# Kernel tuning notes

Hardware: AMD Instinct MI355X
Metric: run time of the kernel (lower is better)

## Reference

```python
import jax, jax.numpy as jnp
import numpy as np

N_HEAD = 16

def setup_inputs() -> dict:
    key = jax.random.key(0)
    k1, k2, k3, k4, k5 = jax.random.split(key, 5)
    B, T, C = 2, 2048, 1024
    scale = 1.0 / np.sqrt(C)
    return {
        "x": jax.random.normal(k1, (B, T, C), dtype=jnp.float32),
        "Wqkv": jax.random.normal(k2, (C, 3 * C), dtype=jnp.float32) * scale,
        "bqkv": jax.random.normal(k3, (3 * C,), dtype=jnp.float32) * 0.02,
        "Wproj": jax.random.normal(k4, (C, C), dtype=jnp.float32) * scale,
        "bproj": jax.random.normal(k5, (C,), dtype=jnp.float32) * 0.02,
    }

def reference(x, Wqkv, bqkv, Wproj, bproj):
    B, T, C = x.shape
    H = N_HEAD
    D = C // H
    # qkv projection, split last dim as (3, H, D): first C cols = q, etc.
    qkv = (x @ Wqkv + bqkv).reshape(B, T, 3, H, D)
    q, k, v = qkv[:, :, 0], qkv[:, :, 1], qkv[:, :, 2]  # (B, T, H, D)
    att = jnp.einsum("bqhd,bkhd->bhqk", q, k) * (1.0 / np.sqrt(D))
    causal = jnp.tril(jnp.ones((T, T), dtype=bool))
    att = jnp.where(causal, att, -jnp.inf)
    att = jax.nn.softmax(att, axis=-1)
    y = jnp.einsum("bhqk,bkhd->bqhd", att, v).reshape(B, T, C)
    return y @ Wproj + bproj
```

## Files before the change

### kernel.cpp

```cpp
#include <hip/hip_runtime.h>
#include <hip/hip_bf16.h>
#include <stdint.h>

typedef unsigned short u16;
typedef __attribute__((ext_vector_type(8))) short bf16x8;
typedef __attribute__((ext_vector_type(4))) float f32x4;

#define MFMA16(a,b,c) __builtin_amdgcn_mfma_f32_16x16x32_bf16((a),(b),(c),0,0,0)

__device__ __forceinline__ u16 f2bf(float f) {
    union { float f; uint32_t u; } v; v.f = f;
    return (u16)((v.u + 0x7FFFu + ((v.u >> 16) & 1u)) >> 16);
}

__global__ void k_convert(const float* __restrict__ in, u16* __restrict__ out) {
    int i = (blockIdx.x * 256 + threadIdx.x) * 4;
    f32x4 v = *(const f32x4*)(in + i);
    uint64_t p = (uint64_t)f2bf(v[0]) | ((uint64_t)f2bf(v[1]) << 16)
               | ((uint64_t)f2bf(v[2]) << 32) | ((uint64_t)f2bf(v[3]) << 48);
    *(uint64_t*)(out + i) = p;
}

__global__ void k_transpose_convert(const float* __restrict__ W, u16* __restrict__ WT,
                                    int R, int NC) {
    int id = blockIdx.x * 256 + threadIdx.x;
    int n = id % NC, kc = id / NC;
    bf16x8 o;
#pragma unroll
    for (int i = 0; i < 8; ++i)
        o[i] = (short)f2bf(W[(size_t)(kc * 8 + i) * NC + n]);
    *(bf16x8*)(WT + (size_t)n * R + kc * 8) = o;
}

__global__ void k_transpose_v(const u16* __restrict__ V, u16* __restrict__ Vt) {
    int id = blockIdx.x * 256 + threadIdx.x;
    int d = id & 63, tc = (id >> 6) & 255, bh = id >> 14;
    const u16* src = V + (size_t)bh * 131072 + d;
    u16* dst = Vt + (size_t)bh * 131072 + (size_t)d * 2048 + tc * 8;
    bf16x8 o;
#pragma unroll
    for (int i = 0; i < 8; ++i) o[i] = (short)src[(size_t)(tc * 8 + i) * 64];
    *(bf16x8*)dst = o;
}

__global__ __launch_bounds__(256, 2) void k_gemm(
    const u16* __restrict__ A, const u16* __restrict__ Bt,
    const float* __restrict__ bias,
    u16* __restrict__ outQKV, float* __restrict__ outF,
    int M, int N, int K, int mode)
{
    __shared__ __align__(16) u16 As[2][128 * 32];
    __shared__ __align__(16) u16 Bs[2][128 * 32];
    const int tid = threadIdx.x;
    const int nbx = N >> 7;
    const int bm = blockIdx.x / nbx, bn = blockIdx.x % nbx;
    const int m0 = bm << 7, n0 = bn << 7;
    const int l = tid & 63, w = tid >> 6;
    const int wr = w >> 1, wc = w & 1;
    const int kl = l >> 4, lr = l & 15;

    const int r0 = tid >> 2, kc0 = tid & 3, r1 = r0 + 64;
    const int wa0 = r0 * 32 + (((kc0 ^ (r0 >> 1)) & 3) << 3);
    const int wa1 = r1 * 32 + (((kc0 ^ (r1 >> 1)) & 3) << 3);
    const size_t ga0 = (size_t)r0 * K + kc0 * 8;
    const size_t ga1 = (size_t)r1 * K + kc0 * 8;
    const u16* Ag = A + (size_t)m0 * K;
    const u16* Bg = Bt + (size_t)n0 * K;

    f32x4 acc[4][4] = {};

    int ra[4], rb[4];
#pragma unroll
    for (int m = 0; m < 4; ++m) {
        int row = wr * 64 + m * 16 + lr;
        ra[m] = row * 32 + (((kl ^ (row >> 1)) & 3) << 3);
    }
#pragma unroll
    for (int n = 0; n < 4; ++n) {
        int row = wc * 64 + n * 16 + lr;
        rb[n] = row * 32 + (((kl ^ (row >> 1)) & 3) << 3);
    }

    {
        bf16x8 a0 = *(const bf16x8*)(Ag + ga0);
        bf16x8 a1 = *(const bf16x8*)(Ag + ga1);
        bf16x8 b0 = *(const bf16x8*)(Bg + ga0);
        bf16x8 b1 = *(const bf16x8*)(Bg + ga1);
        *(bf16x8*)&As[0][wa0] = a0; *(bf16x8*)&As[0][wa1] = a1;
        *(bf16x8*)&Bs[0][wa0] = b0; *(bf16x8*)&Bs[0][wa1] = b1;
    }
    __syncthreads();

    const int nK = K >> 5;
    int cur = 0;
    for (int ks = 0; ks < nK; ++ks) {
        bf16x8 a0, a1, b0, b1;
        const bool pre = (ks + 1 < nK);
        if (pre) {
            size_t off = (size_t)(ks + 1) * 32;
            a0 = *(const bf16x8*)(Ag + ga0 + off);
            a1 = *(const bf16x8*)(Ag + ga1 + off);
            b0 = *(const bf16x8*)(Bg + ga0 + off);
            b1 = *(const bf16x8*)(Bg + ga1 + off);
        }
        bf16x8 af[4], bfr[4];
#pragma unroll
        for (int m = 0; m < 4; ++m) af[m] = *(const bf16x8*)&As[cur][ra[m]];
#pragma unroll
        for (int n = 0; n < 4; ++n) bfr[n] = *(const bf16x8*)&Bs[cur][rb[n]];
#pragma unroll
        for (int m = 0; m < 4; ++m)
#pragma unroll
            for (int n = 0; n < 4; ++n)
                acc[m][n] = MFMA16(af[m], bfr[n], acc[m][n]);
        if (pre) {
            int nxt = cur ^ 1;
            *(bf16x8*)&As[nxt][wa0] = a0; *(bf16x8*)&As[nxt][wa1] = a1;
            *(bf16x8*)&Bs[nxt][wa0] = b0; *(bf16x8*)&Bs[nxt][wa1] = b1;
        }
        __syncthreads();
        cur ^= 1;
    }

    if (mode == 0) {
#pragma unroll
        for (int n = 0; n < 4; ++n) {
            int gn = n0 + wc * 64 + n * 16 + lr;
            float bv = bias[gn];
            int s = gn >> 10, hd = gn & 1023;
            int hh = hd >> 6, dd = hd & 63;
            float mult = (s == 0) ? 0.125f : 1.0f;
            size_t base = (size_t)s * 4194304 + (size_t)hh * 131072 + dd;
#pragma unroll
            for (int m = 0; m < 4; ++m)
#pragma unroll
                for (int j = 0; j < 4; ++j) {
                    int gm = m0 + wr * 64 + m * 16 + kl * 4 + j;
                    int bb = gm >> 11, tt = gm & 2047;
                    float val = (acc[m][n][j] + bv) * mult;
                    outQKV[base + (size_t)bb * 2097152 + (size_t)tt * 64] = f2bf(val);
                }
        }
    } else {
#pragma unroll
        for (int n = 0; n < 4; ++n) {
            int gn = n0 + wc * 64 + n * 16 + lr;
            float bv = bias[gn];
#pragma unroll
            for (int m = 0; m < 4; ++m)
#pragma unroll
                for (int j = 0; j < 4; ++j) {
                    int gm = m0 + wr * 64 + m * 16 + kl * 4 + j;
                    outF[(size_t)gm * N + gn] = acc[m][n][j] + bv;
                }
        }
    }
}

__global__ __launch_bounds__(256, 4) void k_attn(
    const u16* __restrict__ Qg, const u16* __restrict__ Kg,
    const u16* __restrict__ Vtg, u16* __restrict__ Yg)
{
    const int bid = blockIdx.x;
    const int bh = bid & 31;
    const int qt = 31 - (bid >> 5);
    const int b = bh >> 4, h = bh & 15;
    const int q0 = qt << 6;
    const int tid = threadIdx.x, l = tid & 63, w = tid >> 6;
    const int kl = l >> 4, lr = l & 15;

    __shared__ __align__(16) u16 Qs[64 * 64];
    __shared__ __align__(16) u16 Ks[64 * 64];
    __shared__ __align__(16) u16 Vs[64 * 64];
    __shared__ __align__(16) u16 Ps[4][16 * 72];

    const u16* Qb = Qg + (size_t)bh * 131072;
    const u16* Kb = Kg + (size_t)bh * 131072;
    const u16* Vb = Vtg + (size_t)bh * 131072;

    const int rr = tid >> 3, ch = tid & 7;
    {
        bf16x8 a = *(const bf16x8*)(Qb + (size_t)(q0 + rr) * 64 + ch * 8);
        bf16x8 c = *(const bf16x8*)(Qb + (size_t)(q0 + rr + 32) * 64 + ch * 8);
        *(bf16x8*)&Qs[rr * 64 + ((ch ^ (rr & 7)) << 3)] = a;
        *(bf16x8*)&Qs[(rr + 32) * 64 + ((ch ^ (rr & 7)) << 3)] = c;
    }
    __syncthreads();
    bf16x8 qa[2];
#pragma unroll
    for (int kk = 0; kk < 2; ++kk) {
        int row = w * 16 + lr;
        qa[kk] = *(const bf16x8*)&Qs[row * 64 + (((kk * 4 + kl) ^ (row & 7)) << 3)];
    }

    f32x4 oacc[4] = {};
    float lsum[4] = {0.f, 0.f, 0.f, 0.f};

    bf16x8 kv0 = *(const bf16x8*)(Kb + (size_t)rr * 64 + ch * 8);
    bf16x8 kv1 = *(const bf16x8*)(Kb + (size_t)(rr + 32) * 64 + ch * 8);
    bf16x8 vv0 = *(const bf16x8*)(Vb + (size_t)rr * 2048 + ch * 8);
    bf16x8 vv1 = *(const bf16x8*)(Vb + (size_t)(rr + 32) * 2048 + ch * 8);

    for (int kt = 0; kt <= qt; ++kt) {
        const int k0 = kt << 6;
        __syncthreads();
        *(bf16x8*)&Ks[rr * 64 + ((ch ^ (rr & 7)) << 3)] = kv0;
        *(bf16x8*)&Ks[(rr + 32) * 64 + ((ch ^ (rr & 7)) << 3)] = kv1;
        *(bf16x8*)&Vs[rr * 64 + ((ch ^ (rr & 7)) << 3)] = vv0;
        *(bf16x8*)&Vs[(rr + 32) * 64 + ((ch ^ (rr & 7)) << 3)] = vv1;
        __syncthreads();
        if (kt < qt) {
            const int k0n = k0 + 64;
            kv0 = *(const bf16x8*)(Kb + (size_t)(k0n + rr) * 64 + ch * 8);
            kv1 = *(const bf16x8*)(Kb + (size_t)(k0n + rr + 32) * 64 + ch * 8);
            vv0 = *(const bf16x8*)(Vb + (size_t)rr * 2048 + k0n + ch * 8);
            vv1 = *(const bf16x8*)(Vb + (size_t)(rr + 32) * 2048 + k0n + ch * 8);
        }

        f32x4 s[4];
#pragma unroll
        for (int nb = 0; nb < 4; ++nb) {
            f32x4 a = {};
            int key = nb * 16 + lr;
#pragma unroll
            for (int kk = 0; kk < 2; ++kk) {
                bf16x8 kb = *(const bf16x8*)&Ks[key * 64 + (((kk * 4 + kl) ^ (key & 7)) << 3)];
                a = MFMA16(qa[kk], kb, a);
            }
            s[nb] = a;
        }
        if (kt == qt) {
#pragma unroll
            for (int nb = 0; nb < 4; ++nb) {
                int key = k0 + nb * 16 + lr;
#pragma unroll
                for (int j = 0; j < 4; ++j) {
                    int q = q0 + w * 16 + kl * 4 + j;
                    if (key > q) s[nb][j] = -__builtin_inff();
                }
            }
        }
#pragma unroll
        for (int j = 0; j < 4; ++j) {
            float acc4 = 0.f;
#pragma unroll
            for (int nb = 0; nb < 4; ++nb) {
                float p = __expf(s[nb][j]);
                s[nb][j] = p;
                acc4 += p;
            }
            lsum[j] += acc4;
        }
#pragma unroll
        for (int nb = 0; nb < 4; ++nb)
#pragma unroll
            for (int j = 0; j < 4; ++j)
                Ps[w][(kl * 4 + j) * 72 + nb * 16 + lr] = f2bf(s[nb][j]);
        bf16x8 pa[2];
#pragma unroll
        for (int kk = 0; kk < 2; ++kk)
            pa[kk] = *(const bf16x8*)&Ps[w][lr * 72 + kk * 32 + kl * 8];
#pragma unroll
        for (int db = 0; db < 4; ++db) {
            int d = db * 16 + lr;
#pragma unroll
            for (int kk = 0; kk < 2; ++kk) {
                bf16x8 vb = *(const bf16x8*)&Vs[d * 64 + (((kk * 4 + kl) ^ (d & 7)) << 3)];
                oacc[db] = MFMA16(pa[kk], vb, oacc[db]);
            }
        }
    }
#pragma unroll
    for (int j = 0; j < 4; ++j) {
#pragma unroll
        for (int off = 1; off < 16; off <<= 1) lsum[j] += __shfl_xor(lsum[j], off);
        lsum[j] = 1.f / lsum[j];
    }
#pragma unroll
    for (int db = 0; db < 4; ++db)
#pragma unroll
        for (int j = 0; j < 4; ++j) {
            int q = q0 + w * 16 + kl * 4 + j;
            int col = h * 64 + db * 16 + lr;
            Yg[(size_t)(b * 2048 + q) * 1024 + col] = f2bf(oacc[db][j] * lsum[j]);
        }
}

extern "C" void kernel_launch(void* const* d_in, const int* in_sizes, int n_in,
                              void* d_out, int out_size, void* d_ws, size_t ws_size,
                              hipStream_t stream) {
    const float* x     = (const float*)d_in[0];
    const float* Wqkv  = (const float*)d_in[1];
    const float* bqkv  = (const float*)d_in[2];
    const float* Wproj = (const float*)d_in[3];
    const float* bproj = (const float*)d_in[4];
    float* out = (float*)d_out;

    char* ws = (char*)d_ws;
    u16* xb     = (u16*)(ws);
    u16* WqkvT  = (u16*)(ws + 8388608);
    u16* WprojT = (u16*)(ws + 14680064);
    u16* qkv    = (u16*)(ws + 16777216);
    u16* Vt   = xb;
    u16* Yatt = qkv + 2 * 4194304;

    k_convert<<<4096, 256, 0, stream>>>(x, xb);
    k_transpose_convert<<<1536, 256, 0, stream>>>(Wqkv, WqkvT, 1024, 3072);
    k_transpose_convert<<<512, 256, 0, stream>>>(Wproj, WprojT, 1024, 1024);
    k_gemm<<<768, 256, 0, stream>>>(xb, WqkvT, bqkv, qkv, nullptr,
                                    4096, 3072, 1024, 0);
    k_transpose_v<<<2048, 256, 0, stream>>>(qkv + 2 * 4194304, Vt);
    k_attn<<<1024, 256, 0, stream>>>(qkv, qkv + 4194304, Vt, Yatt);
    k_gemm<<<256, 256, 0, stream>>>(Yatt, WprojT, bproj, nullptr, out,
                                    4096, 1024, 1024, 1);
}
```

Measured before the change: 119.8 us.

## Use direct global-to-LDS loads in GEMM and narrow projection tile

The GEMM kernel becomes a template on the number of N-repeats and the output mode. Tiles are now staged with direct global-to-LDS 16-byte loads instead of loading into registers and then storing to LDS. The bank-conflict swizzle moves from the LDS write address to the global read address. The output projection uses a 128x64 tile with twice as many blocks, and both GEMMs declare launch bounds for higher occupancy. The aim is to cut register pressure and VGPR round-trips on the load path and to fill more CUs for the smaller projection GEMM, at the cost of relying on the async LDS load path being ordered correctly by the barriers.

```diff
diff --git a/kernel.cpp b/kernel.cpp
--- a/kernel.cpp
+++ b/kernel.cpp
@@ -43,89 +43,102 @@
     *(bf16x8*)dst = o;
 }
 
-__global__ __launch_bounds__(256, 2) void k_gemm(
+template<int NREP, int MODE>
+__device__ __forceinline__ void gemm_body(
     const u16* __restrict__ A, const u16* __restrict__ Bt,
     const float* __restrict__ bias,
     u16* __restrict__ outQKV, float* __restrict__ outF,
-    int M, int N, int K, int mode)
+    int M, int N, int K)
 {
+    constexpr int BN = 32 * NREP;
+    constexpr int WN = 16 * NREP;
+    constexpr int BSLOTS = NREP / 2;
     __shared__ __align__(16) u16 As[2][128 * 32];
-    __shared__ __align__(16) u16 Bs[2][128 * 32];
+    __shared__ __align__(16) u16 Bs[2][BN * 32];
     const int tid = threadIdx.x;
-    const int nbx = N >> 7;
+    const int nbx = N / BN;
     const int bm = blockIdx.x / nbx, bn = blockIdx.x % nbx;
-    const int m0 = bm << 7, n0 = bn << 7;
+    const int m0 = bm << 7, n0 = bn * BN;
     const int l = tid & 63, w = tid >> 6;
     const int wr = w >> 1, wc = w & 1;
     const int kl = l >> 4, lr = l & 15;
 
-    const int r0 = tid >> 2, kc0 = tid & 3, r1 = r0 + 64;
-    const int wa0 = r0 * 32 + (((kc0 ^ (r0 >> 1)) & 3) << 3);
-    const int wa1 = r1 * 32 + (((kc0 ^ (r1 >> 1)) & 3) << 3);
-    const size_t ga0 = (size_t)r0 * K + kc0 * 8;
-    const size_t ga1 = (size_t)r1 * K + kc0 * 8;
     const u16* Ag = A + (size_t)m0 * K;
     const u16* Bg = Bt + (size_t)n0 * K;
 
-    f32x4 acc[4][4] = {};
-
-    int ra[4], rb[4];
+    int a_src[2], a_dst[2];
+#pragma unroll
+    for (int s = 0; s < 2; ++s) {
+        int cb = w * 128 + s * 64;
+        int c = cb + l;
+        int r = c >> 2, kc = c & 3;
+        a_src[s] = r * K + ((kc ^ ((r >> 1) & 3)) << 3);
+        a_dst[s] = cb << 3;
+    }
+    int b_src[BSLOTS], b_dst[BSLOTS];
+#pragma unroll
+    for (int s = 0; s < BSLOTS; ++s) {
+        int cb = (w * BSLOTS + s) * 64;
+        int c = cb + l;
+        int r = c >> 2, kc = c & 3;
+        b_src[s] = r * K + ((kc ^ ((r >> 1) & 3)) << 3);
+        b_dst[s] = cb << 3;
+    }
+
+    int ra[4], rb[NREP];
 #pragma unroll
     for (int m = 0; m < 4; ++m) {
         int row = wr * 64 + m * 16 + lr;
         ra[m] = row * 32 + (((kl ^ (row >> 1)) & 3) << 3);
     }
 #pragma unroll
-    for (int n = 0; n < 4; ++n) {
-        int row = wc * 64 + n * 16 + lr;
+    for (int n = 0; n < NREP; ++n) {
+        int row = wc * WN + n * 16 + lr;
         rb[n] = row * 32 + (((kl ^ (row >> 1)) & 3) << 3);
     }
 
-    {
-        bf16x8 a0 = *(const bf16x8*)(Ag + ga0);
-        bf16x8 a1 = *(const bf16x8*)(Ag + ga1);
-        bf16x8 b0 = *(const bf16x8*)(Bg + ga0);
-        bf16x8 b1 = *(const bf16x8*)(Bg + ga1);
-        *(bf16x8*)&As[0][wa0] = a0; *(bf16x8*)&As[0][wa1] = a1;
-        *(bf16x8*)&Bs[0][wa0] = b0; *(bf16x8*)&Bs[0][wa1] = b1;
-    }
+    f32x4 acc[4][NREP] = {};
+
+#pragma unroll
+    for (int s = 0; s < 2; ++s)
+        __builtin_amdgcn_global_load_lds(Ag + a_src[s], &As[0][a_dst[s]], 16, 0, 0);
+#pragma unroll
+    for (int s = 0; s < BSLOTS; ++s)
+        __builtin_amdgcn_global_load_lds(Bg + b_src[s], &Bs[0][b_dst[s]], 16, 0, 0);
     __syncthreads();
 
     const int nK = K >> 5;
     int cur = 0;
     for (int ks = 0; ks < nK; ++ks) {
-        bf16x8 a0, a1, b0, b1;
-        const bool pre = (ks + 1 < nK);
-        if (pre) {
-            size_t off = (size_t)(ks + 1) * 32;
-            a0 = *(const bf16x8*)(Ag + ga0 + off);
-            a1 = *(const bf16x8*)(Ag + ga1 + off);
-            b0 = *(const bf16x8*)(Bg + ga0 + off);
-            b1 = *(const bf16x8*)(Bg + ga1 + off);
-        }
-        bf16x8 af[4], bfr[4];
+        if (ks + 1 < nK) {
+            int off = (ks + 1) << 5;
+#pragma unroll
+            for (int s = 0; s < 2; ++s)
+                __builtin_amdgcn_global_load_lds(Ag + a_src[s] + off,
+                                                 &As[cur ^ 1][a_dst[s]], 16, 0, 0);
+#pragma unroll
+            for (int s = 0; s < BSLOTS; ++s)
+                __builtin_amdgcn_global_load_lds(Bg + b_src[s] + off,
+                                                 &Bs[cur ^ 1][b_dst[s]], 16, 0, 0);
+        }
+        bf16x8 af[4], bfr[NREP];
 #pragma unroll
         for (int m = 0; m < 4; ++m) af[m] = *(const bf16x8*)&As[cur][ra[m]];
 #pragma unroll
-        for (int n = 0; n < 4; ++n) bfr[n] = *(const bf16x8*)&Bs[cur][rb[n]];
+        for (int n = 0; n < NREP; ++n) bfr[n] = *(const bf16x8*)&Bs[cur][rb[n]];
 #pragma unroll
         for (int m = 0; m < 4; ++m)
 #pragma unroll
-            for (int n = 0; n < 4; ++n)
+            for (int n = 0; n < NREP; ++n)
                 acc[m][n] = MFMA16(af[m], bfr[n], acc[m][n]);
-        if (pre) {
-            int nxt = cur ^ 1;
-            *(bf16x8*)&As[nxt][wa0] = a0; *(bf16x8*)&As[nxt][wa1] = a1;
-            *(bf16x8*)&Bs[nxt][wa0] = b0; *(bf16x8*)&Bs[nxt][wa1] = b1;
-        }
         __syncthreads();
         cur ^= 1;
     }
 
-    if (mode == 0) {
-#pragma unroll
-        for (int n = 0; n < 4; ++n) {
-            int gn = n0 + wc * 64 + n * 16 + lr;
+    if (MODE == 0) {
+#pragma unroll
+        for (int n = 0; n < NREP; ++n) {
+            int gn = n0 + wc * WN + n * 16 + lr;
             float bv = bias[gn];
             int s = gn >> 10, hd = gn & 1023;
             int hh = hd >> 6, dd = hd & 63;
@@ -143,8 +156,8 @@
         }
     } else {
 #pragma unroll
-        for (int n = 0; n < 4; ++n) {
-            int gn = n0 + wc * 64 + n * 16 + lr;
+        for (int n = 0; n < NREP; ++n) {
+            int gn = n0 + wc * WN + n * 16 + lr;
             float bv = bias[gn];
 #pragma unroll
             for (int m = 0; m < 4; ++m)
@@ -155,6 +168,22 @@
                 }
         }
     }
+}
+
+__global__ __launch_bounds__(256, 4) void k_gemm_qkv(
+    const u16* __restrict__ A, const u16* __restrict__ Bt,
+    const float* __restrict__ bias, u16* __restrict__ outQKV,
+    int M, int N, int K)
+{
+    gemm_body<4, 0>(A, Bt, bias, outQKV, nullptr, M, N, K);
+}
+
+__global__ __launch_bounds__(256, 4) void k_gemm_proj(
+    const u16* __restrict__ A, const u16* __restrict__ Bt,
+    const float* __restrict__ bias, float* __restrict__ outF,
+    int M, int N, int K)
+{
+    gemm_body<2, 1>(A, Bt, bias, nullptr, outF, M, N, K);
 }
 
 __global__ __launch_bounds__(256, 4) void k_attn(
@@ -307,10 +336,10 @@
     k_convert<<<4096, 256, 0, stream>>>(x, xb);
     k_transpose_convert<<<1536, 256, 0, stream>>>(Wqkv, WqkvT, 1024, 3072);
     k_transpose_convert<<<512, 256, 0, stream>>>(Wproj, WprojT, 1024, 1024);
-    k_gemm<<<768, 256, 0, stream>>>(xb, WqkvT, bqkv, qkv, nullptr,
-                                    4096, 3072, 1024, 0);
+    k_gemm_qkv<<<768, 256, 0, stream>>>(xb, WqkvT, bqkv, qkv,
+                                        4096, 3072, 1024);
     k_transpose_v<<<2048, 256, 0, stream>>>(qkv + 2 * 4194304, Vt);
     k_attn<<<1024, 256, 0, stream>>>(qkv, qkv + 4194304, Vt, Yatt);
-    k_gemm<<<256, 256, 0, stream>>>(Yatt, WprojT, bproj, nullptr, out,
-                                    4096, 1024, 1024, 1);
-}
+    k_gemm_proj<<<512, 256, 0, stream>>>(Yatt, WprojT, bproj, out,
+                                         4096, 1024, 1024);
+}
```

Result: no change. 120.6 us (+0.7%).
